# Performance work log

Hardware: AMD Instinct MI355X
Metric: run time of the kernel (lower is better)

## Reference

```python
import jax, jax.numpy as jnp
import numpy as np

B, S, H, D = 2, 512, 32, 128
T = 2048          # max_seq_len (KV cache length)
DM = H * D        # 4096
ROPE_BASE = 10000.0


def setup_inputs() -> dict:
    key = jax.random.key(0)
    ks = jax.random.split(key, 5)
    x = jax.random.normal(ks[0], (B, S, DM), dtype=jnp.float32)
    wqkv = jax.random.normal(ks[1], (3 * DM, DM), dtype=jnp.float32) * 0.02
    wo = jax.random.normal(ks[2], (DM, DM), dtype=jnp.float32) * 0.02
    k_cache = jax.random.normal(ks[3], (B, H, T, D), dtype=jnp.float32)
    v_cache = jax.random.normal(ks[4], (B, H, T, D), dtype=jnp.float32)
    batch_idx = jnp.arange(B, dtype=jnp.int32)
    # prefill chunk written at positions T-S .. T-1
    input_pos = jnp.broadcast_to(jnp.arange(T - S, T, dtype=jnp.int32), (B, S))
    return {"x": x, "wqkv": wqkv, "wo": wo, "k_cache": k_cache,
            "v_cache": v_cache, "batch_idx": batch_idx, "input_pos": input_pos}


def _rope(x, cos, sin):
    # x: [B,S,H,D]; cos/sin: [B,S,D/2]
    xs = x.reshape(*x.shape[:-1], D // 2, 2)
    x0, x1 = xs[..., 0], xs[..., 1]
    c = cos[:, :, None, :]
    s = sin[:, :, None, :]
    out = jnp.stack([x0 * c - x1 * s, x1 * c + x0 * s], axis=-1)
    return out.reshape(x.shape)


def reference(x, wqkv, wo, k_cache, v_cache, batch_idx, input_pos):
    # fused QKV projection (torch Linear: y = x @ W^T)
    qkv = jnp.einsum('bsd,ed->bse', x, wqkv)
    q, k, v = jnp.split(qkv, 3, axis=-1)
    q = q.reshape(B, S, H, D)
    k = k.reshape(B, S, H, D)
    v = v.reshape(B, S, H, D)

    # RoPE at positions input_pos
    inv_freq = 1.0 / (ROPE_BASE ** (jnp.arange(0, D, 2, dtype=jnp.float32) / D))
    ang = input_pos.astype(jnp.float32)[..., None] * inv_freq  # [B,S,D/2]
    cos, sin = jnp.cos(ang), jnp.sin(ang)
    q = _rope(q, cos, sin)
    k = _rope(k, cos, sin)

    # scatter new k/v into caches at [batch_idx, :, input_pos]
    k_cache = k_cache.at[batch_idx[:, None], :, input_pos].set(k)
    v_cache = v_cache.at[batch_idx[:, None], :, input_pos].set(v)

    # causal block-mask over cache positions: kv_pos <= input_pos[q]
    q_bh = q.transpose(0, 2, 1, 3)  # [B,H,S,D]
    scale = 1.0 / jnp.sqrt(jnp.float32(D))
    scores = jnp.einsum('bhsd,bhtd->bhst', q_bh, k_cache) * scale
    kv_pos = jnp.arange(T, dtype=jnp.int32)
    mask = kv_pos[None, None, None, :] <= input_pos[:, None, :, None]  # [B,1,S,T]
    scores = jnp.where(mask, scores, jnp.float32(-1e30))
    attn = jax.nn.softmax(scores, axis=-1)
    y = jnp.einsum('bhst,bhtd->bhsd', attn, v_cache)
    y = y.transpose(0, 2, 1, 3).reshape(B, S, DM)
    return jnp.einsum('bsd,ed->bse', y, wo)
```

## Files before the change

kernel.cpp:

```cpp
#include <hip/hip_runtime.h>
#include <hip/hip_bf16.h>

#define NB 2
#define NS 512
#define NH 32
#define ND 128
#define NT 2048
#define NDM 4096
#define NE 12288

typedef __attribute__((ext_vector_type(4))) float f32x4;
typedef __attribute__((ext_vector_type(8))) short s16x8;
typedef unsigned int u32;

__device__ __forceinline__ short f2bs(float x) {
  unsigned int u = __float_as_uint(x);
  u += 0x7fffu + ((u >> 16) & 1u);
  return (short)(u >> 16);
}
__device__ __forceinline__ float bs2f(short s) {
  return __uint_as_float(((unsigned int)(unsigned short)s) << 16);
}
__device__ __forceinline__ s16x8 cvt8(float4 a, float4 b) {
  s16x8 o;
  o[0] = f2bs(a.x); o[1] = f2bs(a.y); o[2] = f2bs(a.z); o[3] = f2bs(a.w);
  o[4] = f2bs(b.x); o[5] = f2bs(b.y); o[6] = f2bs(b.z); o[7] = f2bs(b.w);
  return o;
}
__device__ __forceinline__ void gl16(const short* g, short* l) {
  __builtin_amdgcn_global_load_lds(
      (const __attribute__((address_space(1))) u32*)g,
      (__attribute__((address_space(3))) u32*)l, 16, 0, 0);
}

__global__ void f2b_kernel(const float* __restrict__ src, short* __restrict__ dst) {
  const size_t i = ((size_t)blockIdx.x * 256 + threadIdx.x) * 8;
  const float4* s = (const float4*)(src + i);
  *(s16x8*)(dst + i) = cvt8(s[0], s[1]);
}

template<bool C_BF16>
__global__ __launch_bounds__(256) void gemm_bt(
    const short* __restrict__ A, const short* __restrict__ B,
    void* __restrict__ Cp, int M, int N, int K)
{
  __shared__ short As[128 * 32];
  __shared__ short Bs[128 * 32];

  const int tid  = threadIdx.x;
  const int lane = tid & 63;
  const int w    = tid >> 6;
  const int wm = (w >> 1) * 64, wn = (w & 1) * 64;
  const int m0 = blockIdx.y * 128, n0 = blockIdx.x * 128;
  const int lr = lane & 15, lko = (lane >> 4) * 8;
  const int srow = lane >> 2, scol = (lane & 3) * 8;

  const short* ga = A + (size_t)(m0 + w * 32 + srow) * K + scol;
  const short* gb = B + (size_t)(n0 + w * 32 + srow) * K + scol;
  short* la = &As[(w * 32 + srow) * 32 + scol];
  short* lb = &Bs[(w * 32 + srow) * 32 + scol];
  const size_t rstep = (size_t)16 * K;

  f32x4 acc[4][4] = {};
  const int ktiles = K / 32;
  for (int kt = 0; kt < ktiles; ++kt) {
    const int ko = kt * 32;
    gl16(ga + ko,         la);
    gl16(ga + rstep + ko, la + 16 * 32);
    gl16(gb + ko,         lb);
    gl16(gb + rstep + ko, lb + 16 * 32);
    __syncthreads();

    s16x8 af[4], bf[4];
    #pragma unroll
    for (int i = 0; i < 4; ++i) {
      af[i] = *(const s16x8*)&As[(wm + i * 16 + lr) * 32 + lko];
      bf[i] = *(const s16x8*)&Bs[(wn + i * 16 + lr) * 32 + lko];
    }
    #pragma unroll
    for (int mi = 0; mi < 4; ++mi)
      #pragma unroll
      for (int ni = 0; ni < 4; ++ni)
        acc[mi][ni] = __builtin_amdgcn_mfma_f32_16x16x32_bf16(
            af[mi], bf[ni], acc[mi][ni], 0, 0, 0);
    __syncthreads();
  }

  #pragma unroll
  for (int mi = 0; mi < 4; ++mi) {
    const int r0 = m0 + wm + mi * 16 + (lane >> 4) * 4;
    #pragma unroll
    for (int ni = 0; ni < 4; ++ni) {
      const int c = n0 + wn + ni * 16 + lr;
      const f32x4 v = acc[mi][ni];
      #pragma unroll
      for (int j = 0; j < 4; ++j) {
        if constexpr (C_BF16)
          ((short*)Cp)[(size_t)(r0 + j) * N + c] = f2bs(v[j]);
        else
          ((float*)Cp)[(size_t)(r0 + j) * N + c] = v[j];
      }
    }
  }
}

template<bool A_BF16, bool C_BF16>
__global__ __launch_bounds__(256, 2) void gemm_nt(
    const void* __restrict__ Ap, const float* __restrict__ Bp,
    void* __restrict__ Cp, int M, int N, int K)
{
  constexpr int LP = 40;
  __shared__ short As[2][128][LP];
  __shared__ short Bs[2][128][LP];

  const int tid  = threadIdx.x;
  const int lane = tid & 63;
  const int wv   = tid >> 6;
  const int wm   = (wv >> 1) * 64, wn = (wv & 1) * 64;
  const int m0   = blockIdx.y * 128, n0 = blockIdx.x * 128;
  const int srow = tid >> 1, scol = (tid & 1) * 16;
  const int lr   = lane & 15, lko = (lane >> 4) * 8;

  const float* Af = (const float*)Ap;
  const short* Ab = (const short*)Ap;
  const size_t aOff = (size_t)(m0 + srow) * K + scol;
  const size_t bOff = (size_t)(n0 + srow) * K + scol;

  f32x4 acc[4][4] = {};

  if constexpr (A_BF16) {
    const s16x8* s = (const s16x8*)(Ab + aOff);
    *(s16x8*)&As[0][srow][scol]     = s[0];
    *(s16x8*)&As[0][srow][scol + 8] = s[1];
  } else {
    const float4* s = (const float4*)(Af + aOff);
    *(s16x8*)&As[0][srow][scol]     = cvt8(s[0], s[1]);
    *(s16x8*)&As[0][srow][scol + 8] = cvt8(s[2], s[3]);
  }
  {
    const float4* s = (const float4*)(Bp + bOff);
    *(s16x8*)&Bs[0][srow][scol]     = cvt8(s[0], s[1]);
    *(s16x8*)&Bs[0][srow][scol + 8] = cvt8(s[2], s[3]);
  }
  __syncthreads();

  const int ktiles = K / 32;
  for (int kt = 0; kt < ktiles; ++kt) {
    const int cur = kt & 1;
    const bool has = (kt + 1) < ktiles;
    float4 pa0, pa1, pa2, pa3, pb0, pb1, pb2, pb3;
    s16x8 qa0, qa1;
    if (has) {
      const int k1 = (kt + 1) * 32;
      if constexpr (A_BF16) {
        const s16x8* s = (const s16x8*)(Ab + aOff + k1);
        qa0 = s[0]; qa1 = s[1];
      } else {
        const float4* s = (const float4*)(Af + aOff + k1);
        pa0 = s[0]; pa1 = s[1]; pa2 = s[2]; pa3 = s[3];
      }
      const float4* s = (const float4*)(Bp + bOff + k1);
      pb0 = s[0]; pb1 = s[1]; pb2 = s[2]; pb3 = s[3];
    }
    s16x8 af[4], bf[4];
    #pragma unroll
    for (int i = 0; i < 4; ++i) {
      af[i] = *(const s16x8*)&As[cur][wm + i * 16 + lr][lko];
      bf[i] = *(const s16x8*)&Bs[cur][wn + i * 16 + lr][lko];
    }
    #pragma unroll
    for (int mi = 0; mi < 4; ++mi)
      #pragma unroll
      for (int ni = 0; ni < 4; ++ni)
        acc[mi][ni] = __builtin_amdgcn_mfma_f32_16x16x32_bf16(
            af[mi], bf[ni], acc[mi][ni], 0, 0, 0);
    if (has) {
      const int nxt = cur ^ 1;
      if constexpr (A_BF16) {
        *(s16x8*)&As[nxt][srow][scol]     = qa0;
        *(s16x8*)&As[nxt][srow][scol + 8] = qa1;
      } else {
        *(s16x8*)&As[nxt][srow][scol]     = cvt8(pa0, pa1);
        *(s16x8*)&As[nxt][srow][scol + 8] = cvt8(pa2, pa3);
      }
      *(s16x8*)&Bs[nxt][srow][scol]     = cvt8(pb0, pb1);
      *(s16x8*)&Bs[nxt][srow][scol + 8] = cvt8(pb2, pb3);
    }
    __syncthreads();
  }

  #pragma unroll
  for (int mi = 0; mi < 4; ++mi) {
    const int r0 = m0 + wm + mi * 16 + (lane >> 4) * 4;
    #pragma unroll
    for (int ni = 0; ni < 4; ++ni) {
      const int c = n0 + wn + ni * 16 + lr;
      const f32x4 v = acc[mi][ni];
      #pragma unroll
      for (int j = 0; j < 4; ++j) {
        if constexpr (C_BF16)
          ((short*)Cp)[(size_t)(r0 + j) * N + c] = f2bs(v[j]);
        else
          ((float*)Cp)[(size_t)(r0 + j) * N + c] = v[j];
      }
    }
  }
}

__global__ void copyk_kernel(const float* __restrict__ src, short* __restrict__ dst) {
  const size_t i = ((size_t)blockIdx.x * 256 + threadIdx.x) * 8;
  const float4* s = (const float4*)(src + i);
  *(s16x8*)(dst + i) = cvt8(s[0], s[1]);
}

__global__ __launch_bounds__(256) void vtrans_kernel(
    const float* __restrict__ vc, short* __restrict__ VT)
{
  __shared__ float tile[64][68];
  const int tid = threadIdx.x;
  const size_t bh = blockIdx.z;
  const int tt = blockIdx.x * 64;
  const int dd = blockIdx.y * 64;
  const int row = tid >> 2, c0 = (tid & 3) * 16;
  const float* src = vc + (bh * NT + tt + row) * ND + dd + c0;
  #pragma unroll
  for (int j = 0; j < 4; ++j)
    *(float4*)&tile[row][c0 + j * 4] = *(const float4*)(src + j * 4);
  __syncthreads();
  short tmp[16];
  #pragma unroll
  for (int i = 0; i < 16; ++i) tmp[i] = f2bs(tile[c0 + i][row]);
  short* dst = VT + (bh * ND + dd + row) * NT + tt + c0;
  *(s16x8*)dst       = *(s16x8*)&tmp[0];
  *(s16x8*)(dst + 8) = *(s16x8*)&tmp[8];
}

__global__ __launch_bounds__(256) void rope_kernel(
    const short* __restrict__ qkv, const int* __restrict__ ipos,
    const int* __restrict__ bidx, short* __restrict__ Qr,
    short* __restrict__ Kf, short* __restrict__ VT)
{
  const int bs = blockIdx.x;
  const int b = bs >> 9, s = bs & 511;
  const int tid = threadIdx.x;
  const int h = tid >> 3, r = tid & 7;
  const int pos = ipos[bs];
  const int bi = bidx[b];
  const short* base = qkv + (size_t)bs * NE + h * ND + r * 16;
  const s16x8 q0 = *(const s16x8*)(base);
  const s16x8 q1 = *(const s16x8*)(base + 8);
  const s16x8 k0 = *(const s16x8*)(base + NDM);
  const s16x8 k1 = *(const s16x8*)(base + NDM + 8);
  const s16x8 v0 = *(const s16x8*)(base + 2 * NDM);
  const s16x8 v1 = *(const s16x8*)(base + 2 * NDM + 8);
  const float scale = 0.08838834764831845f;
  s16x8 qo0, qo1, ko0, ko1;
  #pragma unroll
  for (int i = 0; i < 8; ++i) {
    const int d2 = r * 8 + i;
    const float invf = expf(-0.14391156831f * (float)d2);
    const float ang = (float)pos * invf;
    float sn, cs;
    sincosf(ang, &sn, &cs);
    float x0, x1, y0, y1;
    if (i < 4) {
      x0 = bs2f(q0[2 * i]); x1 = bs2f(q0[2 * i + 1]);
      y0 = bs2f(k0[2 * i]); y1 = bs2f(k0[2 * i + 1]);
    } else {
      x0 = bs2f(q1[2 * i - 8]); x1 = bs2f(q1[2 * i - 7]);
      y0 = bs2f(k1[2 * i - 8]); y1 = bs2f(k1[2 * i - 7]);
    }
    const short oq0 = f2bs((x0 * cs - x1 * sn) * scale);
    const short oq1 = f2bs((x1 * cs + x0 * sn) * scale);
    const short ok0 = f2bs(y0 * cs - y1 * sn);
    const short ok1 = f2bs(y1 * cs + y0 * sn);
    if (i < 4) { qo0[2*i]=oq0; qo0[2*i+1]=oq1; ko0[2*i]=ok0; ko0[2*i+1]=ok1; }
    else       { qo1[2*i-8]=oq0; qo1[2*i-7]=oq1; ko1[2*i-8]=ok0; ko1[2*i-7]=ok1; }
  }
  short* qdst = Qr + (((size_t)b * NH + h) * NS + s) * ND + r * 16;
  *(s16x8*)qdst = qo0; *(s16x8*)(qdst + 8) = qo1;
  short* kdst = Kf + (((size_t)bi * NH + h) * NT + pos) * ND + r * 16;
  *(s16x8*)kdst = ko0; *(s16x8*)(kdst + 8) = ko1;
  short* vdst = VT + (((size_t)bi * NH + h) * ND + r * 16) * NT + pos;
  #pragma unroll
  for (int i = 0; i < 16; ++i) {
    const short vv = (i < 8) ? v0[i] : v1[i - 8];
    vdst[(size_t)i * NT] = vv;
  }
}

__global__ __launch_bounds__(256, 2) void attn_kernel(
    const short* __restrict__ Q, const short* __restrict__ Kf,
    const short* __restrict__ VT, const int* __restrict__ ipos,
    short* __restrict__ Y)
{
  __shared__ short Ks[64][136];
  __shared__ short Vs[128][72];
  __shared__ short Ps[128][72];
  __shared__ int pos_sh[128];
  __shared__ int maxpos_sh;

  const int tid = threadIdx.x;
  const int lane = tid & 63;
  const int w = tid >> 6;
  const int s0 = blockIdx.x * 128;
  const int h = blockIdx.y;
  const int b = blockIdx.z;
  const int lr = lane & 15, lg = lane >> 4, lko = lg * 8;

  if (tid < 128) pos_sh[tid] = ipos[b * NS + s0 + tid];
  __syncthreads();
  if (tid == 0) {
    int m = 0;
    for (int i = 0; i < 128; ++i) m = (pos_sh[i] > m) ? pos_sh[i] : m;
    maxpos_sh = m;
  }
  __syncthreads();
  const int maxpos = maxpos_sh;

  const size_t bh = (size_t)b * NH + h;
  const short* Qp = Q + (bh * NS + s0 + w * 32) * ND;
  s16x8 qf[2][4];
  #pragma unroll
  for (int mi = 0; mi < 2; ++mi)
    #pragma unroll
    for (int kc = 0; kc < 4; ++kc)
      qf[mi][kc] = *(const s16x8*)(Qp + (size_t)(mi * 16 + lr) * ND + kc * 32 + lko);

  int prow[2][4];
  float mrun[2][4], lrun[2][4];
  #pragma unroll
  for (int mi = 0; mi < 2; ++mi)
    #pragma unroll
    for (int j = 0; j < 4; ++j) {
      prow[mi][j] = pos_sh[w * 32 + mi * 16 + lg * 4 + j];
      mrun[mi][j] = -1e30f;
      lrun[mi][j] = 0.f;
    }
  f32x4 yac[2][8] = {};

  const short* Kbase = Kf + bh * NT * ND;
  const short* Vbase = VT + bh * ND * NT;
  const int krow = tid >> 2, kc0 = (tid & 3) * 32;
  const int vrow = tid >> 1, vc0 = (tid & 1) * 32;
  const int ntl = maxpos / 64 + 1;

  for (int t = 0; t < ntl; ++t) {
    const int t0 = t * 64;
    {
      const short* src = Kbase + (size_t)(t0 + krow) * ND + kc0;
      #pragma unroll
      for (int j = 0; j < 4; ++j)
        *(s16x8*)&Ks[krow][kc0 + j * 8] = *(const s16x8*)(src + j * 8);
      const short* vsrc = Vbase + (size_t)vrow * NT + t0 + vc0;
      #pragma unroll
      for (int j = 0; j < 4; ++j)
        *(s16x8*)&Vs[vrow][vc0 + j * 8] = *(const s16x8*)(vsrc + j * 8);
    }
    __syncthreads();

    f32x4 sac[2][4] = {};
    #pragma unroll
    for (int kc = 0; kc < 4; ++kc) {
      s16x8 kfr[4];
      #pragma unroll
      for (int ni = 0; ni < 4; ++ni)
        kfr[ni] = *(const s16x8*)&Ks[ni * 16 + lr][kc * 32 + lko];
      #pragma unroll
      for (int mi = 0; mi < 2; ++mi)
        #pragma unroll
        for (int ni = 0; ni < 4; ++ni)
          sac[mi][ni] = __builtin_amdgcn_mfma_f32_16x16x32_bf16(
              qf[mi][kc], kfr[ni], sac[mi][ni], 0, 0, 0);
    }

    #pragma unroll
    for (int mi = 0; mi < 2; ++mi) {
      float alpha[4];
      #pragma unroll
      for (int j = 0; j < 4; ++j) {
        const int rp = prow[mi][j];
        float mv = -1e30f;
        #pragma unroll
        for (int ni = 0; ni < 4; ++ni) {
          float sv = sac[mi][ni][j];
          if (t0 + ni * 16 + lr > rp) sv = -1e30f;
          sac[mi][ni][j] = sv;
          mv = fmaxf(mv, sv);
        }
        #pragma unroll
        for (int off = 1; off < 16; off <<= 1)
          mv = fmaxf(mv, __shfl_xor(mv, off, 64));
        const float mo = mrun[mi][j];
        const float mn = fmaxf(mo, mv);
        const float a = __expf(mo - mn);
        mrun[mi][j] = mn;
        float rs = 0.f;
        #pragma unroll
        for (int ni = 0; ni < 4; ++ni) {
          const float p = __expf(sac[mi][ni][j] - mn);
          sac[mi][ni][j] = p;
          rs += p;
        }
        #pragma unroll
        for (int off = 1; off < 16; off <<= 1)
          rs += __shfl_xor(rs, off, 64);
        lrun[mi][j] = lrun[mi][j] * a + rs;
        alpha[j] = a;
      }
      #pragma unroll
      for (int nn = 0; nn < 8; ++nn)
        #pragma unroll
        for (int j = 0; j < 4; ++j)
          yac[mi][nn][j] *= alpha[j];
      #pragma unroll
      for (int ni = 0; ni < 4; ++ni)
        #pragma unroll
        for (int j = 0; j < 4; ++j)
          Ps[w * 32 + mi * 16 + lg * 4 + j][ni * 16 + lr] = f2bs(sac[mi][ni][j]);
    }
    __syncthreads();

    #pragma unroll
    for (int kc = 0; kc < 2; ++kc) {
      s16x8 vf[8];
      #pragma unroll
      for (int nn = 0; nn < 8; ++nn)
        vf[nn] = *(const s16x8*)&Vs[nn * 16 + lr][kc * 32 + lko];
      #pragma unroll
      for (int mi = 0; mi < 2; ++mi) {
        const s16x8 pf = *(const s16x8*)&Ps[w * 32 + mi * 16 + lr][kc * 32 + lko];
        #pragma unroll
        for (int nn = 0; nn < 8; ++nn)
          yac[mi][nn] = __builtin_amdgcn_mfma_f32_16x16x32_bf16(
              pf, vf[nn], yac[mi][nn], 0, 0, 0);
      }
    }
    __syncthreads();
  }

  #pragma unroll
  for (int mi = 0; mi < 2; ++mi)
    #pragma unroll
    for (int j = 0; j < 4; ++j) {
      const float inv = 1.0f / lrun[mi][j];
      const int srow = s0 + w * 32 + mi * 16 + lg * 4 + j;
      short* yp = Y + ((size_t)b * NS + srow) * NDM + h * ND;
      #pragma unroll
      for (int nn = 0; nn < 8; ++nn)
        yp[nn * 16 + lr] = f2bs(yac[mi][nn][j] * inv);
    }
}

extern "C" void kernel_launch(void* const* d_in, const int* in_sizes, int n_in,
                              void* d_out, int out_size, void* d_ws, size_t ws_size,
                              hipStream_t stream)
{
  (void)in_sizes; (void)n_in; (void)out_size;
  const float* x    = (const float*)d_in[0];
  const float* wqkv = (const float*)d_in[1];
  const float* wo   = (const float*)d_in[2];
  const float* kc   = (const float*)d_in[3];
  const float* vc   = (const float*)d_in[4];
  const int*   bidx = (const int*)d_in[5];
  const int*   ipos = (const int*)d_in[6];
  float* out = (float*)d_out;

  char* ws = (char*)d_ws;
  short* qkv = (short*)(ws);
  short* Qr  = (short*)(ws + 25165824ull);
  short* Kf  = (short*)(ws + 33554432ull);
  short* VT  = (short*)(ws + 67108864ull);
  short* Y   = qkv;
  short* xb  = Qr;
  short* wb  = (short*)(ws + 100663296ull);

  const size_t WS_NEEDED = 201326592ull;

  if (ws_size >= WS_NEEDED) {
    f2b_kernel<<<dim3(2048),  256, 0, stream>>>(x, xb);
    f2b_kernel<<<dim3(24576), 256, 0, stream>>>(wqkv, wb);
    gemm_bt<true><<<dim3(NE / 128, (NB * NS) / 128), 256, 0, stream>>>(
        xb, wb, qkv, NB * NS, NE, NDM);
    copyk_kernel<<<dim3(8192), 256, 0, stream>>>(kc, Kf);
    vtrans_kernel<<<dim3(NT / 64, ND / 64, NB * NH), 256, 0, stream>>>(vc, VT);
    rope_kernel<<<dim3(NB * NS), 256, 0, stream>>>(qkv, ipos, bidx, Qr, Kf, VT);
    attn_kernel<<<dim3(NS / 128, NH, NB), 256, 0, stream>>>(Qr, Kf, VT, ipos, Y);
    f2b_kernel<<<dim3(8192), 256, 0, stream>>>(wo, wb);
    gemm_bt<false><<<dim3(NDM / 128, (NB * NS) / 128), 256, 0, stream>>>(
        Y, wb, out, NB * NS, NDM, NDM);
  } else {
    gemm_nt<false, true><<<dim3(NE / 128, (NB * NS) / 128), 256, 0, stream>>>(
        x, wqkv, qkv, NB * NS, NE, NDM);
    copyk_kernel<<<dim3(8192), 256, 0, stream>>>(kc, Kf);
    vtrans_kernel<<<dim3(NT / 64, ND / 64, NB * NH), 256, 0, stream>>>(vc, VT);
    rope_kernel<<<dim3(NB * NS), 256, 0, stream>>>(qkv, ipos, bidx, Qr, Kf, VT);
    attn_kernel<<<dim3(NS / 128, NH, NB), 256, 0, stream>>>(Qr, Kf, VT, ipos, Y);
    gemm_nt<true, false><<<dim3(NDM / 128, (NB * NS) / 128), 256, 0, stream>>>(
        Y, wo, out, NB * NS, NDM, NDM);
  }
}
```

Before: 473.8 us.

## Replace QKV projection GEMM with 256x256 eight-wave multi-stage pipelined kernel

Adds a new bf16 GEMM kernel with 256x256 output tiles, 8 waves per block, and a 4-slot LDS ring loaded via global_load_lds with XOR-swizzled layout. Loads for upcoming k-slices are issued while MFMAs run, using explicit vmcnt waits, barriers and setprio. It is used only for the QKV projection (M=1024, N=12288, K=4096), replacing the 128x128 tile kernel. Larger tiles raise data reuse but give only 192 blocks, which lowers occupancy and wave-level parallelism.

```diff
diff --git a/kernel.cpp b/kernel.cpp
--- a/kernel.cpp
+++ b/kernel.cpp
@@ -37,6 +37,100 @@
   const size_t i = ((size_t)blockIdx.x * 256 + threadIdx.x) * 8;
   const float4* s = (const float4*)(src + i);
   *(s16x8*)(dst + i) = cvt8(s[0], s[1]);
+}
+
+__global__ __launch_bounds__(512, 2) void gemm8p(
+    const short* __restrict__ A, const short* __restrict__ B,
+    short* __restrict__ C, int M, int N, int K)
+{
+  __shared__ short ldsA[4 * 8192];
+  __shared__ short ldsB[4 * 8192];
+
+  const int tid = threadIdx.x;
+  const int l   = tid & 63;
+  const int w   = tid >> 6;
+  const int wm  = w >> 2, wn = w & 3;
+  const int m0  = blockIdx.y * 256, n0 = blockIdx.x * 256;
+  const int nhalf = (K / 32) * 2;
+
+  auto STAGE = [&](int s) {
+    const int op    = s & 1;
+    const int sigma = s >> 1;
+    const int slot  = sigma & 3;
+    const int k0    = sigma * 32;
+    short* region   = (op ? ldsB : ldsA) + slot * 8192;
+    const short* g  = op ? B : A;
+    const int base0 = op ? n0 : m0;
+    #pragma unroll
+    for (int c = 0; c < 2; ++c) {
+      const int o    = c * 8192 + tid * 16;
+      const int line = o >> 7;
+      const int off  = (o & 127) ^ ((line & 7) << 4);
+      const int r    = (line << 1) | (off >> 6);
+      const int cb   = off & 63;
+      gl16(g + (size_t)(base0 + r) * K + k0 + (cb >> 1), region + (o >> 1));
+    }
+  };
+
+  auto FRAG = [&](const short* ring, int slot, int r) -> s16x8 {
+    const int cb   = (l >> 4) << 4;
+    const int line = r >> 1;
+    const int off  = (((r & 1) << 6) | cb) ^ ((line & 7) << 4);
+    return *(const s16x8*)((const char*)(ring + slot * 8192) + (line << 7) + off);
+  };
+
+  f32x4 acc[8][4] = {};
+
+  for (int s = 0; s < 6; ++s) STAGE(s);
+  asm volatile("s_waitcnt vmcnt(4)" ::: "memory");
+  __builtin_amdgcn_s_barrier();
+
+  const int ktiles = K / 64;
+  for (int j = 0; j < ktiles; ++j) {
+    s16x8 bfr[4];
+    #pragma unroll
+    for (int q = 0; q < 4; ++q) {
+      const int kk = q >> 1, mh = q & 1;
+      const int slot = (2 * j + kk) & 3;
+      s16x8 af[4];
+      #pragma unroll
+      for (int i = 0; i < 4; ++i)
+        af[i] = FRAG(ldsA, slot, wm * 128 + (mh * 4 + i) * 16 + (l & 15));
+      if (mh == 0) {
+        #pragma unroll
+        for (int i = 0; i < 4; ++i)
+          bfr[i] = FRAG(ldsB, slot, wn * 64 + i * 16 + (l & 15));
+      }
+      const int s = 4 * j + q + 6;
+      if (s < nhalf) STAGE(s);
+      __builtin_amdgcn_s_barrier();
+      __builtin_amdgcn_s_setprio(1);
+      #pragma unroll
+      for (int i = 0; i < 4; ++i)
+        #pragma unroll
+        for (int nf = 0; nf < 4; ++nf)
+          acc[mh * 4 + i][nf] = __builtin_amdgcn_mfma_f32_16x16x32_bf16(
+              af[i], bfr[nf], acc[mh * 4 + i][nf], 0, 0, 0);
+      __builtin_amdgcn_s_setprio(0);
+      if (q == 3) {
+        if (j < ktiles - 2)       asm volatile("s_waitcnt vmcnt(4)" ::: "memory");
+        else if (j == ktiles - 2) asm volatile("s_waitcnt vmcnt(0)" ::: "memory");
+      }
+      __builtin_amdgcn_s_barrier();
+    }
+  }
+
+  #pragma unroll
+  for (int mf = 0; mf < 8; ++mf) {
+    const int r0 = m0 + wm * 128 + mf * 16 + (l >> 4) * 4;
+    #pragma unroll
+    for (int nf = 0; nf < 4; ++nf) {
+      const int cc = n0 + wn * 64 + nf * 16 + (l & 15);
+      #pragma unroll
+      for (int jj = 0; jj < 4; ++jj)
+        C[(size_t)(r0 + jj) * N + cc] = f2bs(acc[mf][nf][jj]);
+    }
+  }
 }
 
 template<bool C_BF16>
@@ -480,7 +574,7 @@
   if (ws_size >= WS_NEEDED) {
     f2b_kernel<<<dim3(2048),  256, 0, stream>>>(x, xb);
     f2b_kernel<<<dim3(24576), 256, 0, stream>>>(wqkv, wb);
-    gemm_bt<true><<<dim3(NE / 128, (NB * NS) / 128), 256, 0, stream>>>(
+    gemm8p<<<dim3(NE / 256, (NB * NS) / 256), 512, 0, stream>>>(
         xb, wb, qkv, NB * NS, NE, NDM);
     copyk_kernel<<<dim3(8192), 256, 0, stream>>>(kc, Kf);
     vtrans_kernel<<<dim3(NT / 64, ND / 64, NB * NH), 256, 0, stream>>>(vc, VT);
```

Measured after the change: 465.5 us. About the same (-1.8%).

## Fuse weight fp32-to-bf16 conversion into double-buffered swizzled GEMM

Applied to the files above, without the earlier changes.

The GEMM now reads fp32 weights directly, converting them to bf16 in registers as it writes them to shared memory. This removes the separate f2b passes over wqkv and wo and the extra weight workspace. The main loop is double-buffered, with register prefetch of B and async LDS loads of A. It also adds an XOR-swizzled LDS layout, barrier-only sync and raised priority around the MFMAs. The cost is that each block reads fp32 weights per tile and converts them again, doubling B-side global traffic versus pre-converted bf16.

```diff
diff --git a/kernel.cpp b/kernel.cpp
--- a/kernel.cpp
+++ b/kernel.cpp
@@ -40,50 +40,117 @@
 }
 
 template<bool C_BF16>
-__global__ __launch_bounds__(256) void gemm_bt(
-    const short* __restrict__ A, const short* __restrict__ B,
+__global__ __launch_bounds__(256, 2) void gemm_btf(
+    const short* __restrict__ A, const float* __restrict__ B,
     void* __restrict__ Cp, int M, int N, int K)
 {
-  __shared__ short As[128 * 32];
-  __shared__ short Bs[128 * 32];
+  __shared__ short ldsA[2][4096];
+  __shared__ short ldsB[2][4096];
 
   const int tid  = threadIdx.x;
   const int lane = tid & 63;
   const int w    = tid >> 6;
   const int wm = (w >> 1) * 64, wn = (w & 1) * 64;
   const int m0 = blockIdx.y * 128, n0 = blockIdx.x * 128;
-  const int lr = lane & 15, lko = (lane >> 4) * 8;
-  const int srow = lane >> 2, scol = (lane & 3) * 8;
-
-  const short* ga = A + (size_t)(m0 + w * 32 + srow) * K + scol;
-  const short* gb = B + (size_t)(n0 + w * 32 + srow) * K + scol;
-  short* la = &As[(w * 32 + srow) * 32 + scol];
-  short* lb = &Bs[(w * 32 + srow) * 32 + scol];
-  const size_t rstep = (size_t)16 * K;
+  const int lr  = lane & 15;
+  const int fcb = (lane >> 4) << 4;
+
+  const int rB  = tid >> 1;
+  const int cB0 = (tid & 1) * 16;
+  const float* gB = B + (size_t)(n0 + rB) * K + cB0;
+
+  auto stageA = [&](int kt, int buf) {
+    const int k0 = kt * 32;
+    #pragma unroll
+    for (int c = 0; c < 2; ++c) {
+      const int o    = c * 4096 + tid * 16;
+      const int line = o >> 7;
+      const int off  = (o & 127) ^ ((line & 7) << 4);
+      const int r    = (line << 1) | (off >> 6);
+      const int cb   = off & 63;
+      gl16(A + (size_t)(m0 + r) * K + k0 + (cb >> 1), &ldsA[buf][o >> 1]);
+    }
+  };
+  auto loadB = [&](int kt, float4* reg) {
+    const float* s = gB + kt * 32;
+    #pragma unroll
+    for (int c = 0; c < 4; ++c) reg[c] = *(const float4*)(s + c * 4);
+  };
+  auto writeB = [&](int buf, const float4* reg) {
+    #pragma unroll
+    for (int half = 0; half < 2; ++half) {
+      const int cb   = cB0 * 2 + half * 16;
+      const int line = rB >> 1;
+      const int off  = (((rB & 1) << 6) | cb) ^ ((line & 7) << 4);
+      *(s16x8*)((char*)ldsB[buf] + (line << 7) + off) =
+          cvt8(reg[half * 2], reg[half * 2 + 1]);
+    }
+  };
+  auto fragA = [&](int buf, int r) -> s16x8 {
+    const int line = r >> 1;
+    const int off  = (((r & 1) << 6) | fcb) ^ ((line & 7) << 4);
+    return *(const s16x8*)((const char*)ldsA[buf] + (line << 7) + off);
+  };
+  auto fragB = [&](int buf, int r) -> s16x8 {
+    const int line = r >> 1;
+    const int off  = (((r & 1) << 6) | fcb) ^ ((line & 7) << 4);
+    return *(const s16x8*)((const char*)ldsB[buf] + (line << 7) + off);
+  };
 
   f32x4 acc[4][4] = {};
+  float4 bregA[4], bregB[4];
+
+  stageA(0, 0);
+  loadB(0, bregA);
+
   const int ktiles = K / 32;
-  for (int kt = 0; kt < ktiles; ++kt) {
-    const int ko = kt * 32;
-    gl16(ga + ko,         la);
-    gl16(ga + rstep + ko, la + 16 * 32);
-    gl16(gb + ko,         lb);
-    gl16(gb + rstep + ko, lb + 16 * 32);
-    __syncthreads();
-
-    s16x8 af[4], bf[4];
-    #pragma unroll
-    for (int i = 0; i < 4; ++i) {
-      af[i] = *(const s16x8*)&As[(wm + i * 16 + lr) * 32 + lko];
-      bf[i] = *(const s16x8*)&Bs[(wn + i * 16 + lr) * 32 + lko];
-    }
-    #pragma unroll
-    for (int mi = 0; mi < 4; ++mi)
-      #pragma unroll
-      for (int ni = 0; ni < 4; ++ni)
-        acc[mi][ni] = __builtin_amdgcn_mfma_f32_16x16x32_bf16(
-            af[mi], bf[ni], acc[mi][ni], 0, 0, 0);
-    __syncthreads();
+  for (int kt = 0; kt < ktiles; kt += 2) {
+    stageA(kt + 1, 1);
+    loadB(kt + 1, bregB);
+    writeB(0, bregA);
+    asm volatile("s_waitcnt lgkmcnt(0)" ::: "memory");
+    __builtin_amdgcn_s_barrier();
+    {
+      s16x8 af[4], bf[4];
+      #pragma unroll
+      for (int i = 0; i < 4; ++i) {
+        af[i] = fragA(0, wm + i * 16 + lr);
+        bf[i] = fragB(0, wn + i * 16 + lr);
+      }
+      __builtin_amdgcn_s_setprio(1);
+      #pragma unroll
+      for (int mi = 0; mi < 4; ++mi)
+        #pragma unroll
+        for (int ni = 0; ni < 4; ++ni)
+          acc[mi][ni] = __builtin_amdgcn_mfma_f32_16x16x32_bf16(
+              af[mi], bf[ni], acc[mi][ni], 0, 0, 0);
+      __builtin_amdgcn_s_setprio(0);
+    }
+    __builtin_amdgcn_s_barrier();
+    if (kt + 2 < ktiles) {
+      stageA(kt + 2, 0);
+      loadB(kt + 2, bregA);
+    }
+    writeB(1, bregB);
+    asm volatile("s_waitcnt lgkmcnt(0)" ::: "memory");
+    __builtin_amdgcn_s_barrier();
+    {
+      s16x8 af[4], bf[4];
+      #pragma unroll
+      for (int i = 0; i < 4; ++i) {
+        af[i] = fragA(1, wm + i * 16 + lr);
+        bf[i] = fragB(1, wn + i * 16 + lr);
+      }
+      __builtin_amdgcn_s_setprio(1);
+      #pragma unroll
+      for (int mi = 0; mi < 4; ++mi)
+        #pragma unroll
+        for (int ni = 0; ni < 4; ++ni)
+          acc[mi][ni] = __builtin_amdgcn_mfma_f32_16x16x32_bf16(
+              af[mi], bf[ni], acc[mi][ni], 0, 0, 0);
+      __builtin_amdgcn_s_setprio(0);
+    }
+    __builtin_amdgcn_s_barrier();
   }
 
   #pragma unroll
@@ -473,22 +540,19 @@
   short* VT  = (short*)(ws + 67108864ull);
   short* Y   = qkv;
   short* xb  = Qr;
-  short* wb  = (short*)(ws + 100663296ull);
-
-  const size_t WS_NEEDED = 201326592ull;
+
+  const size_t WS_NEEDED = 100663296ull;
 
   if (ws_size >= WS_NEEDED) {
-    f2b_kernel<<<dim3(2048),  256, 0, stream>>>(x, xb);
-    f2b_kernel<<<dim3(24576), 256, 0, stream>>>(wqkv, wb);
-    gemm_bt<true><<<dim3(NE / 128, (NB * NS) / 128), 256, 0, stream>>>(
-        xb, wb, qkv, NB * NS, NE, NDM);
+    f2b_kernel<<<dim3(2048), 256, 0, stream>>>(x, xb);
+    gemm_btf<true><<<dim3(NE / 128, (NB * NS) / 128), 256, 0, stream>>>(
+        xb, wqkv, qkv, NB * NS, NE, NDM);
     copyk_kernel<<<dim3(8192), 256, 0, stream>>>(kc, Kf);
     vtrans_kernel<<<dim3(NT / 64, ND / 64, NB * NH), 256, 0, stream>>>(vc, VT);
     rope_kernel<<<dim3(NB * NS), 256, 0, stream>>>(qkv, ipos, bidx, Qr, Kf, VT);
     attn_kernel<<<dim3(NS / 128, NH, NB), 256, 0, stream>>>(Qr, Kf, VT, ipos, Y);
-    f2b_kernel<<<dim3(8192), 256, 0, stream>>>(wo, wb);
-    gemm_bt<false><<<dim3(NDM / 128, (NB * NS) / 128), 256, 0, stream>>>(
-        Y, wb, out, NB * NS, NDM, NDM);
+    gemm_btf<false><<<dim3(NDM / 128, (NB * NS) / 128), 256, 0, stream>>>(
+        Y, wo, out, NB * NS, NDM, NDM);
   } else {
     gemm_nt<false, true><<<dim3(NE / 128, (NB * NS) / 128), 256, 0, stream>>>(
         x, wqkv, qkv, NB * NS, NE, NDM);
```

Measured after the change: 515.5 us. 1.09x slower.
